# Optimization experiments

Measured on AMD Instinct MI355X. Metric: run time of the kernel, lower is better.

## Reference

```python
import jax, jax.numpy as jnp
import numpy as np

N_HEAD = 16


def setup_inputs() -> dict:
    key = jax.random.key(0)
    ks = jax.random.split(key, 6)
    B, T, H = 4, 2048, 1024
    inp = jax.random.normal(ks[0], (B, T, H), dtype=jnp.float32)
    # padding mask: valid prefix of random length in [T//2, T] per batch row
    lengths = jax.random.randint(ks[1], (B, 1), T // 2, T + 1)
    mask = jnp.arange(T)[None, :] < lengths  # (B, T) bool
    s = 0.02
    w_qkv = jax.random.normal(ks[2], (H, 3 * H), dtype=jnp.float32) * s
    b_qkv = jax.random.normal(ks[3], (3 * H,), dtype=jnp.float32) * s
    w_out = jax.random.normal(ks[4], (H, H), dtype=jnp.float32) * s
    b_out = jax.random.normal(ks[5], (H,), dtype=jnp.float32) * s
    return {"input": inp, "mask": mask, "w_qkv": w_qkv, "b_qkv": b_qkv,
            "w_out": w_out, "b_out": b_out}


def reference(input, mask, w_qkv, b_qkv, w_out, b_out):
    B, T, H = input.shape
    hd = H // N_HEAD
    qkv = input @ w_qkv + b_qkv                       # (B, T, 3H)
    q, k, v = jnp.split(qkv, 3, axis=-1)
    # (B, T, H) -> (B, nh, T, hd)
    q = q.reshape(B, T, N_HEAD, hd).transpose(0, 2, 1, 3)
    k = k.reshape(B, T, N_HEAD, hd).transpose(0, 2, 1, 3)
    v = v.reshape(B, T, N_HEAD, hd).transpose(0, 2, 1, 3)
    scores = jnp.einsum('bhqd,bhkd->bhqk', q, k) / jnp.sqrt(jnp.float32(hd))
    causal = jnp.tril(jnp.ones((T, T), dtype=bool))   # (T, T)
    full_mask = causal[None, None, :, :] & mask[:, None, None, :]  # (B,1,T,T) bcast over heads
    scores = jnp.where(full_mask, scores, -jnp.inf)
    attn = jax.nn.softmax(scores, axis=-1)            # (B, nh, T, T)
    o = jnp.einsum('bhqk,bhkd->bhqd', attn, v)        # (B, nh, T, hd)
    o = o.transpose(0, 2, 1, 3).reshape(B, T, H)
    return o @ w_out + b_out
```

## Files before the change

### kernel.cpp

```cpp
#include <hip/hip_runtime.h>
#include <math.h>

#define B_  4
#define T_  2048
#define H_  1024
#define NH  16
#define HD  64
#define H3  3072

typedef short bf16x8 __attribute__((ext_vector_type(8)));
typedef short bf16x4 __attribute__((ext_vector_type(4)));
typedef float f32x4  __attribute__((ext_vector_type(4)));
typedef float f32x16 __attribute__((ext_vector_type(16)));

#define SC2F 0.18033688011112042f

__device__ __forceinline__ unsigned short f2bf(float f) {
    union { float f; unsigned u; } v; v.f = f;
    unsigned u = v.u;
    unsigned r = (u + 0x7fffu + ((u >> 16) & 1u)) >> 16;
    return (unsigned short)r;
}

__device__ __forceinline__ void gload_lds16(const void* g, void* l) {
    __builtin_amdgcn_global_load_lds(
        (const __attribute__((address_space(1))) unsigned*)g,
        (__attribute__((address_space(3))) unsigned*)l, 16, 0, 0);
}

__device__ __forceinline__ f32x4 mfma_16x16x16_bf16(bf16x4 a, bf16x4 b, f32x4 c) {
#if __has_builtin(__builtin_amdgcn_mfma_f32_16x16x16_bf16)
    return __builtin_amdgcn_mfma_f32_16x16x16_bf16(a, b, c, 0, 0, 0);
#elif __has_builtin(__builtin_amdgcn_mfma_f32_16x16x16bf16_1k)
    return __builtin_amdgcn_mfma_f32_16x16x16bf16_1k(a, b, c, 0, 0, 0);
#else
    f32x4 d;
    asm volatile("v_mfma_f32_16x16x16_bf16 %0, %1, %2, %3"
                 : "=v"(d) : "v"(a), "v"(b), "v"(c));
    return d;
#endif
}

__global__ void lengths_kernel(const void* mask, int* lengths) {
    int b = blockIdx.x;
    int t = threadIdx.x;
    const unsigned* mu = (const unsigned*)mask;
    bool is_byte = (mu[0] == 0x01010101u);
    int cnt = 0;
    if (is_byte) {
        const unsigned char* m8 = (const unsigned char*)mask;
        for (int i = t; i < T_; i += 256) cnt += (m8[b * T_ + i] != 0);
    } else {
        const unsigned* m32 = (const unsigned*)mask;
        for (int i = t; i < T_; i += 256) cnt += (m32[b * T_ + i] != 0);
    }
    __shared__ int red[256];
    red[t] = cnt;
    __syncthreads();
    for (int s = 128; s > 0; s >>= 1) {
        if (t < s) red[t] += red[t + s];
        __syncthreads();
    }
    if (t == 0) lengths[b] = red[0];
}

__global__ void convert_bf16_kernel(const float* __restrict__ x,
                                    unsigned short* __restrict__ y, int n) {
    int i = (blockIdx.x * 256 + threadIdx.x) * 4;
    if (i < n) {
        float4 v = *(const float4*)(x + i);
        ushort4 o;
        o.x = f2bf(v.x); o.y = f2bf(v.y); o.z = f2bf(v.z); o.w = f2bf(v.w);
        *(ushort4*)(y + i) = o;
    }
}

__global__ void transpose2_kernel(const float* __restrict__ Wqkv,
                                  unsigned short* __restrict__ WqkvT,
                                  const float* __restrict__ Wout,
                                  unsigned short* __restrict__ WoutT) {
    __shared__ unsigned short tile[32][33];
    const int K = H_;
    const float* in;
    unsigned short* out;
    int N, nb;
    if (blockIdx.x < 96) { in = Wqkv; out = WqkvT; N = H3; nb = blockIdx.x * 32; }
    else                 { in = Wout; out = WoutT; N = H_; nb = (blockIdx.x - 96) * 32; }
    int kb = blockIdx.y * 32;
    int tx = threadIdx.x, ty = threadIdx.y;
    for (int i = 0; i < 32; i += 8)
        tile[ty + i][tx] = f2bf(in[(long)(kb + ty + i) * N + nb + tx]);
    __syncthreads();
    for (int i = 0; i < 32; i += 8)
        out[(long)(nb + ty + i) * K + kb + tx] = tile[tx][ty + i];
}

template <int TN, bool BF16_OUT, bool KSCALE, bool VSPLIT>
__global__ __launch_bounds__(256) void gemm_kernel(
    const unsigned short* __restrict__ A,
    const unsigned short* __restrict__ Bt,
    const float* __restrict__ bias,
    void* __restrict__ C,
    unsigned short* __restrict__ Vt,
    int M, int N, int K)
{
    __shared__ unsigned short Asm[2][128][64];
    __shared__ unsigned short Bsm[2][TN][64];

    int nbx = gridDim.x;
    int bid = blockIdx.y * nbx + blockIdx.x;
    int cpx = (nbx * gridDim.y) >> 3;
    int lin = (bid & 7) * cpx + (bid >> 3);
    int bx = lin % nbx, by = lin / nbx;

    int tn = bx * TN, tm = by * 128;
    int tid = threadIdx.x;
    int wid = tid >> 6, lane = tid & 63;
    int l31 = lane & 31, lh = lane >> 5;
    int wm = (wid & 1) * 64, wn = (wid >> 1) * (TN / 2);

    int rl = lane >> 3;
    int g8 = ((lane & 7) ^ rl) * 8;
    const unsigned short* aP = A  + (long)(tm + wid * 32 + rl) * K + g8;
    const unsigned short* bP = Bt + (long)(tn + wid * (TN / 4) + rl) * K + g8;
    int rk = l31 & 7;

    f32x16 acc[2][TN / 64] = {};

#pragma unroll
    for (int t = 0; t < 4; t++)
        gload_lds16(aP + (long)(t * 8) * K, &Asm[0][wid * 32 + t * 8][0]);
#pragma unroll
    for (int t = 0; t < TN / 32; t++)
        gload_lds16(bP + (long)(t * 8) * K, &Bsm[0][wid * (TN / 4) + t * 8][0]);

    int cur = 0;
    for (int k0 = 0; k0 < K; k0 += 64) {
        __syncthreads();

        if (k0 + 64 < K) {
#pragma unroll
            for (int t = 0; t < 4; t++)
                gload_lds16(aP + (long)(t * 8) * K + k0 + 64, &Asm[cur ^ 1][wid * 32 + t * 8][0]);
#pragma unroll
            for (int t = 0; t < TN / 32; t++)
                gload_lds16(bP + (long)(t * 8) * K + k0 + 64, &Bsm[cur ^ 1][wid * (TN / 4) + t * 8][0]);
        }

#pragma unroll
        for (int ks = 0; ks < 4; ks++) {
            int pc = ((ks * 2 + lh) ^ rk) * 8;
            bf16x8 af[2], bv[TN / 64];
            af[0] = *(const bf16x8*)(&Asm[cur][wm + l31][pc]);
            af[1] = *(const bf16x8*)(&Asm[cur][wm + 32 + l31][pc]);
#pragma unroll
            for (int j = 0; j < TN / 64; j++)
                bv[j] = *(const bf16x8*)(&Bsm[cur][wn + j * 32 + l31][pc]);
#pragma unroll
            for (int i = 0; i < 2; i++)
#pragma unroll
                for (int j = 0; j < TN / 64; j++)
                    acc[i][j] = __builtin_amdgcn_mfma_f32_32x32x16_bf16(
                        af[i], bv[j], acc[i][j], 0, 0, 0);
        }
        cur ^= 1;
    }

    if (VSPLIT && tn >= 2 * H_) {
#pragma unroll
        for (int i = 0; i < 2; i++)
#pragma unroll
            for (int j = 0; j < TN / 64; j++) {
                int col = tn + wn + j * 32 + l31;
                float bs = bias[col];
                int feat = col - 2 * H_;
#pragma unroll
                for (int rg = 0; rg < 4; rg++) {
                    int tok0 = tm + wm + i * 32 + rg * 8 + lh * 4;
                    int bb = tok0 >> 11;
                    unsigned d0 = (unsigned)f2bf(acc[i][j][rg * 4 + 0] + bs) |
                                  ((unsigned)f2bf(acc[i][j][rg * 4 + 1] + bs) << 16);
                    unsigned d1 = (unsigned)f2bf(acc[i][j][rg * 4 + 2] + bs) |
                                  ((unsigned)f2bf(acc[i][j][rg * 4 + 3] + bs) << 16);
                    unsigned short* dst = Vt + ((long)(bb * 1024 + feat)) * T_ + (tok0 & (T_ - 1));
                    *(uint2*)dst = make_uint2(d0, d1);
                }
            }
        return;
    }

#pragma unroll
    for (int i = 0; i < 2; i++)
#pragma unroll
        for (int j = 0; j < TN / 64; j++) {
            int col = tn + wn + j * 32 + l31;
            float bs = bias[col];
            bool ks_ = KSCALE && (col >= H_) && (col < 2 * H_);
#pragma unroll
            for (int r = 0; r < 16; r++) {
                int row = tm + wm + i * 32 + (r & 3) + 8 * (r >> 2) + 4 * lh;
                float v = acc[i][j][r] + bs;
                if (ks_) v *= SC2F;
                if (BF16_OUT)
                    ((unsigned short*)C)[(long)row * N + col] = f2bf(v);
                else
                    ((float*)C)[(long)row * N + col] = v;
            }
        }
}

__global__ __launch_bounds__(256) void attn_kernel(
    const unsigned short* __restrict__ QKV,
    const unsigned short* __restrict__ Vt,
    const int* __restrict__ lengths,
    unsigned short* __restrict__ O)
{
    int idx = blockIdx.x;
    int bh = idx & 63;
    int qt = 15 - (idx >> 6);
    int b = bh >> 4, h = bh & 15;
    int len = lengths[b];
    int q0 = qt * 128;

    int tid = threadIdx.x;
    int wid = tid >> 6, lane = tid & 63, quad = lane >> 4, lr = lane & 15;
    int quad4 = quad * 4;

    __shared__ __align__(16) unsigned short SH[16384];
    unsigned short (*Kd)[64][64] = (unsigned short (*)[64][64])(&SH[0]);
    unsigned short (*Vd)[64][64] = (unsigned short (*)[64][64])(&SH[8192]);

    const long qkv_base = (long)b * T_ * H3;

    bf16x8 qf[2][2];
#pragma unroll
    for (int nq = 0; nq < 2; nq++)
#pragma unroll
        for (int ks = 0; ks < 2; ks++)
            qf[nq][ks] = *(const bf16x8*)(QKV + qkv_base +
                (long)(q0 + wid * 32 + nq * 16 + lr) * H3 + h * HD + ks * 32 + quad * 8);

    int rl = lane >> 3;
    int g8 = ((lane & 7) ^ rl) * 8;
    const unsigned short* kB = QKV + qkv_base + (long)(wid * 16 + rl) * H3 + H_ + h * HD + g8;
    const unsigned short* vB = Vt + (long)(bh * 64 + wid * 16 + rl) * T_ + g8;

    f32x4 lacc[2] = {};
    f32x4 Oacc[4][2] = {};

    int kmax = min(q0 + 127, len - 1);
    int n_kt = (kmax >> 6) + 1;
    int q_wave_lo = q0 + wid * 32;
    int qwl_u = __builtin_amdgcn_readfirstlane(q_wave_lo);
    int q_wave_hi = qwl_u + 31;
    int bnd_[2] = { min(q_wave_lo + lr, len - 1),
                    min(q_wave_lo + 16 + lr, len - 1) };
    int rk = lr & 7;

    const short oneb = (short)0x3F80;
    bf16x4 vones = { oneb, oneb, oneb, oneb };

#pragma unroll
    for (int t = 0; t < 2; t++) {
        gload_lds16(kB + (long)(t * 8) * H3, &Kd[0][wid * 16 + t * 8][0]);
        gload_lds16(vB + (long)(t * 8) * T_, &Vd[0][wid * 16 + t * 8][0]);
    }

    for (int kt = 0; kt < n_kt; kt++) {
        int cur = kt & 1;
        __syncthreads();

        if (kt + 1 < n_kt) {
            long koff = (long)((kt + 1) * 64) * H3;
            int voff = (kt + 1) * 64;
#pragma unroll
            for (int t = 0; t < 2; t++) {
                gload_lds16(kB + koff + (long)(t * 8) * H3, &Kd[cur ^ 1][wid * 16 + t * 8][0]);
                gload_lds16(vB + (long)(t * 8) * T_ + voff, &Vd[cur ^ 1][wid * 16 + t * 8][0]);
            }
        }

        int k_lo = kt * 64;
        if (k_lo > q_wave_hi || k_lo >= len) continue;

        int mt_hi = min(q_wave_hi, len - 1);
        int nmt = min(4, ((mt_hi - k_lo) >> 4) + 1);
        nmt = __builtin_amdgcn_readfirstlane(nmt);

        f32x4 Sacc[4][2] = {};
        __builtin_amdgcn_s_setprio(1);
#pragma unroll
        for (int mt = 0; mt < 4; mt++) {
            if (mt >= nmt) continue;
#pragma unroll
            for (int ks = 0; ks < 2; ks++) {
                bf16x8 kf = *(const bf16x8*)(&Kd[cur][mt * 16 + lr][((ks * 4 + quad) ^ rk) * 8]);
                Sacc[mt][0] = __builtin_amdgcn_mfma_f32_16x16x32_bf16(kf, qf[0][ks], Sacc[mt][0], 0, 0, 0);
                Sacc[mt][1] = __builtin_amdgcn_mfma_f32_16x16x32_bf16(kf, qf[1][ks], Sacc[mt][1], 0, 0, 0);
            }
        }
        __builtin_amdgcn_s_setprio(0);

        unsigned pkk[4][2][2];
#pragma unroll
        for (int mt = 0; mt < 4; mt++) {
            if (mt >= nmt) continue;
            int kb0 = k_lo + mt * 16;
            int kbl = kb0 + quad4;
#pragma unroll
            for (int nq = 0; nq < 2; nq++) {
                float p[4];
                if (kb0 + 15 <= qwl_u + nq * 16 && kb0 + 15 < len) {
#pragma unroll
                    for (int r = 0; r < 4; r++)
                        p[r] = __builtin_amdgcn_exp2f(Sacc[mt][nq][r]);
                } else {
                    int dlt = bnd_[nq] - kbl;
#pragma unroll
                    for (int r = 0; r < 4; r++) {
                        float s = (r <= dlt) ? Sacc[mt][nq][r] : -INFINITY;
                        p[r] = __builtin_amdgcn_exp2f(s);
                    }
                }
                pkk[mt][nq][0] = __builtin_amdgcn_perm(__float_as_uint(p[1]), __float_as_uint(p[0]), 0x07060302);
                pkk[mt][nq][1] = __builtin_amdgcn_perm(__float_as_uint(p[3]), __float_as_uint(p[2]), 0x07060302);
            }
        }

        __builtin_amdgcn_s_setprio(1);
#pragma unroll
        for (int mt = 0; mt < 4; mt++) {
            if (mt >= nmt) continue;
            union { unsigned u[2]; bf16x4 v; } bu[2];
            bu[0].u[0] = pkk[mt][0][0]; bu[0].u[1] = pkk[mt][0][1];
            bu[1].u[0] = pkk[mt][1][0]; bu[1].u[1] = pkk[mt][1][1];
            lacc[0] = mfma_16x16x16_bf16(vones, bu[0].v, lacc[0]);
            lacc[1] = mfma_16x16x16_bf16(vones, bu[1].v, lacc[1]);
#pragma unroll
            for (int md = 0; md < 4; md++) {
                bf16x4 vf = *(const bf16x4*)(&Vd[cur][md * 16 + lr]
                    [((mt * 2 + (quad >> 1)) ^ rk) * 8 + (quad & 1) * 4]);
                Oacc[md][0] = mfma_16x16x16_bf16(vf, bu[0].v, Oacc[md][0]);
                Oacc[md][1] = mfma_16x16x16_bf16(vf, bu[1].v, Oacc[md][1]);
            }
        }
        __builtin_amdgcn_s_setprio(0);
    }

    __syncthreads();
    {
        unsigned short (*Es)[68] = (unsigned short (*)[68])(&SH[0]);
        float inv[2] = { 1.f / lacc[0][0], 1.f / lacc[1][0] };
#pragma unroll
        for (int nq = 0; nq < 2; nq++)
#pragma unroll
            for (int md = 0; md < 4; md++)
#pragma unroll
                for (int rp = 0; rp < 2; rp++) {
                    float e0 = Oacc[md][nq][rp * 2]     * inv[nq];
                    float e1 = Oacc[md][nq][rp * 2 + 1] * inv[nq];
                    unsigned w = __builtin_amdgcn_perm(__float_as_uint(e1), __float_as_uint(e0), 0x07060302);
                    *(unsigned*)(&Es[wid * 32 + nq * 16 + lr][md * 16 + quad * 4 + rp * 2]) = w;
                }
        __asm__ volatile("s_waitcnt lgkmcnt(0)" ::: "memory");
        int row = lane >> 1, cb = (lane & 1) * 32;
        long tok = (long)b * T_ + q0 + wid * 32 + row;
#pragma unroll
        for (int i = 0; i < 4; i++) {
            float4 v = *(const float4*)(&Es[wid * 32 + row][cb + i * 8]);
            *(float4*)(&O[tok * H_ + h * HD + cb + i * 8]) = v;
        }
    }
}

extern "C" void kernel_launch(void* const* d_in, const int* in_sizes, int n_in,
                              void* d_out, int out_size, void* d_ws, size_t ws_size,
                              hipStream_t stream) {
    const float* X    = (const float*)d_in[0];
    const void*  mask = d_in[1];
    const float* Wqkv = (const float*)d_in[2];
    const float* bqkv = (const float*)d_in[3];
    const float* Wout = (const float*)d_in[4];
    const float* bout = (const float*)d_in[5];

    char* ws = (char*)d_ws;
    int* lengths          = (int*)ws;
    unsigned short* WqkvT = (unsigned short*)(ws + 256);
    unsigned short* WoutT = WqkvT + (long)H3 * H_;
    unsigned short* QKV   = WoutT + (long)H_ * H_;
    unsigned short* Xbf   = QKV + (long)B_ * T_ * H3;
    unsigned short* Vt    = Xbf + (long)B_ * T_ * H_;
    unsigned short* Obf   = Xbf;

    const int M = B_ * T_;

    lengths_kernel<<<B_, 256, 0, stream>>>(mask, lengths);
    convert_bf16_kernel<<<(M * H_ / 4 + 255) / 256, 256, 0, stream>>>(X, Xbf, M * H_);
    transpose2_kernel<<<dim3(128, H_ / 32), dim3(32, 8), 0, stream>>>(Wqkv, WqkvT, Wout, WoutT);
    gemm_kernel<128, true, true, true><<<dim3(H3 / 128, M / 128), 256, 0, stream>>>(
        Xbf, WqkvT, bqkv, QKV, Vt, M, H3, H_);
    attn_kernel<<<B_ * NH * (T_ / 128), 256, 0, stream>>>(QKV, Vt, lengths, Obf);
    gemm_kernel<64, false, false, false><<<dim3(H_ / 64, M / 128), 256, 0, stream>>>(
        Obf, WoutT, bout, d_out, nullptr, M, H_, H_);
}
```

Measured before the change: 269.9 us.

## Add 256x256 ping-pong scheduled GEMM kernel for the QKV projection

Measured after the change: 278.4 us. +3.1%, slower.

```diff
diff --git a/kernel.cpp b/kernel.cpp
--- a/kernel.cpp
+++ b/kernel.cpp
@@ -95,13 +95,151 @@
         out[(long)(nb + ty + i) * K + kb + tx] = tile[tx][ty + i];
 }
 
-template <int TN, bool BF16_OUT, bool KSCALE, bool VSPLIT>
+#define SPRIO1 __builtin_amdgcn_s_setprio(1)
+#define SPRIO0 __builtin_amdgcn_s_setprio(0)
+#define MIDBAR do { __builtin_amdgcn_sched_barrier(0); __builtin_amdgcn_s_barrier(); \
+    asm volatile("s_waitcnt lgkmcnt(0)" ::: "memory"); __builtin_amdgcn_sched_barrier(0); } while (0)
+#define ENDBAR do { __builtin_amdgcn_sched_barrier(0); __builtin_amdgcn_s_barrier(); \
+    __builtin_amdgcn_sched_barrier(0); } while (0)
+
+__global__ __launch_bounds__(512, 2) void gemm256_kernel(
+    const unsigned short* __restrict__ A,
+    const unsigned short* __restrict__ Bt,
+    const float* __restrict__ bias,
+    unsigned short* __restrict__ C,
+    unsigned short* __restrict__ Vt)
+{
+    const int K = 1024;
+    __shared__ unsigned short As[2][128][64];
+    __shared__ unsigned short Bs[2][128][64];
+
+    int bid = blockIdx.y * 12 + blockIdx.x;
+    int lin = (bid & 7) * 48 + (bid >> 3);
+    int bx = lin % 12, by = lin / 12;
+    int tn = bx * 256, tm = by * 256;
+
+    int tid = threadIdx.x;
+    int wid = tid >> 6, lane = tid & 63;
+    int l31 = lane & 31, lh = lane >> 5;
+    int wr = wid >> 2, wc = wid & 3;
+
+    int rl = lane >> 3;
+    int g  = (lane & 7) ^ rl;
+    const unsigned short* aP = A  + (long)(tm + (wid & 3) * 16 + (wid >> 2) * 128
+                                           + 2 * rl + (g >> 2)) * K + (g & 3) * 8;
+    const unsigned short* bP = Bt + (long)(tn + (wid >> 1) * 64 + (wid & 1) * 16
+                                           + 2 * rl + (g >> 2)) * K + (g & 3) * 8;
+    int awb = (wid & 3) * 8 + (wid >> 2) * 64;
+    int bwb = (wid >> 1) * 32 + (wid & 1) * 8;
+
+#define STG_A(bf, mq, kel) gload_lds16(aP + (long)(mq) * 64 * K + (kel), &As[bf][(mq) * 32 + awb][0])
+#define STG_B(bf, nq, kel) gload_lds16(bP + (long)(nq) * 32 * K + (kel), &Bs[bf][(nq) * 16 + bwb][0])
+
+    int rA  = (l31 >> 1) & 7;
+    int pc0 = (((l31 & 1) * 4) + lh) ^ rA;
+    int aR  = wr * 64 + (l31 >> 1);
+    int bR  = wc * 32 + (l31 >> 1);
+
+#define LD_A(dst, bf, mq) do { \
+    dst[0][0] = *(const bf16x8*)(&As[bf][aR + (mq) * 32][pc0 * 8]); \
+    dst[0][1] = *(const bf16x8*)(&As[bf][aR + (mq) * 32][(pc0 ^ 2) * 8]); \
+    dst[1][0] = *(const bf16x8*)(&As[bf][aR + (mq) * 32 + 16][pc0 * 8]); \
+    dst[1][1] = *(const bf16x8*)(&As[bf][aR + (mq) * 32 + 16][(pc0 ^ 2) * 8]); } while (0)
+#define LD_B(dst, bf, nq) do { \
+    dst[0] = *(const bf16x8*)(&Bs[bf][bR + (nq) * 16][pc0 * 8]); \
+    dst[1] = *(const bf16x8*)(&Bs[bf][bR + (nq) * 16][(pc0 ^ 2) * 8]); } while (0)
+#define MM(mq, af_, nq, bv_) do { \
+    _Pragma("unroll") for (int mf = 0; mf < 2; mf++) \
+    _Pragma("unroll") for (int kk = 0; kk < 2; kk++) \
+        acc[mq][mf][nq] = __builtin_amdgcn_mfma_f32_32x32x16_bf16( \
+            af_[mf][kk], bv_[kk], acc[mq][mf][nq], 0, 0, 0); } while (0)
+
+    f32x16 acc[2][2][2] = {};
+
+    STG_A(0, 0, 0); STG_B(0, 0, 0); STG_A(0, 1, 0); STG_B(0, 1, 0);
+    asm volatile("s_waitcnt vmcnt(2)" ::: "memory");
+    __builtin_amdgcn_sched_barrier(0);
+    STG_A(1, 0, 32); STG_B(1, 0, 32); STG_A(1, 1, 32);
+    asm volatile("s_waitcnt vmcnt(3)" ::: "memory");
+    __builtin_amdgcn_sched_barrier(0);
+    __builtin_amdgcn_s_barrier();
+
+    bf16x8 afA[2][2], afB[2][2], bvA[2], bvB[2];
+
+    for (int it = 0; it < 16; ++it) {
+        bool fl = (it < 15);
+        int kE = it * 64;
+        int kO = kE + 32;
+        int kE2 = kE + 64;
+        int kO2 = kE + 96;
+
+        LD_A(afA, 0, 0); LD_B(bvA, 0, 0);
+        STG_B(1, 1, kO);
+        MIDBAR; SPRIO1; MM(0, afA, 0, bvA); SPRIO0; ENDBAR;
+        LD_A(afB, 0, 1);
+        if (fl) STG_A(0, 0, kE2);
+        MIDBAR; SPRIO1; MM(1, afB, 0, bvA); SPRIO0; ENDBAR;
+        LD_B(bvB, 0, 1);
+        if (fl) STG_B(0, 0, kE2);
+        MIDBAR; SPRIO1; MM(0, afA, 1, bvB); SPRIO0; ENDBAR;
+        if (fl) { STG_A(0, 1, kE2); asm volatile("s_waitcnt vmcnt(3)" ::: "memory"); }
+        else    { asm volatile("s_waitcnt vmcnt(0)" ::: "memory"); }
+        MIDBAR; SPRIO1; MM(1, afB, 1, bvB); SPRIO0; ENDBAR;
+        LD_A(afA, 1, 0); LD_B(bvA, 1, 0);
+        if (fl) STG_B(0, 1, kE2);
+        MIDBAR; SPRIO1; MM(0, afA, 0, bvA); SPRIO0; ENDBAR;
+        LD_A(afB, 1, 1);
+        if (fl) STG_A(1, 0, kO2);
+        MIDBAR; SPRIO1; MM(1, afB, 0, bvA); SPRIO0; ENDBAR;
+        LD_B(bvB, 1, 1);
+        if (fl) STG_B(1, 0, kO2);
+        MIDBAR; SPRIO1; MM(0, afA, 1, bvB); SPRIO0; ENDBAR;
+        if (fl) { STG_A(1, 1, kO2); asm volatile("s_waitcnt vmcnt(3)" ::: "memory"); }
+        MIDBAR; SPRIO1; MM(1, afB, 1, bvB); SPRIO0; ENDBAR;
+    }
+
+    bool vsplit = (tn >= 2 * H_);
+#pragma unroll
+    for (int mq = 0; mq < 2; mq++)
+#pragma unroll
+        for (int mf = 0; mf < 2; mf++)
+#pragma unroll
+            for (int nq = 0; nq < 2; nq++) {
+                int col = tn + wc * 64 + nq * 32 + l31;
+                float bs = bias[col];
+                int rbase = tm + wr * 128 + mq * 64 + mf * 32;
+                if (vsplit) {
+                    int feat = col - 2 * H_;
+#pragma unroll
+                    for (int rg = 0; rg < 4; rg++) {
+                        int tok0 = rbase + rg * 8 + lh * 4;
+                        int bb = tok0 >> 11;
+                        unsigned d0 = (unsigned)f2bf(acc[mq][mf][nq][rg * 4 + 0] + bs) |
+                                      ((unsigned)f2bf(acc[mq][mf][nq][rg * 4 + 1] + bs) << 16);
+                        unsigned d1 = (unsigned)f2bf(acc[mq][mf][nq][rg * 4 + 2] + bs) |
+                                      ((unsigned)f2bf(acc[mq][mf][nq][rg * 4 + 3] + bs) << 16);
+                        unsigned short* dst = Vt + ((long)(bb * 1024 + feat)) * T_ + (tok0 & (T_ - 1));
+                        *(uint2*)dst = make_uint2(d0, d1);
+                    }
+                } else {
+                    bool ks_ = (col >= H_) && (col < 2 * H_);
+#pragma unroll
+                    for (int r = 0; r < 16; r++) {
+                        int row = rbase + (r & 3) + 8 * (r >> 2) + 4 * lh;
+                        float v = acc[mq][mf][nq][r] + bs;
+                        if (ks_) v *= SC2F;
+                        C[(long)row * H3 + col] = f2bf(v);
+                    }
+                }
+            }
+}
+
+template <int TN>
 __global__ __launch_bounds__(256) void gemm_kernel(
     const unsigned short* __restrict__ A,
     const unsigned short* __restrict__ Bt,
     const float* __restrict__ bias,
-    void* __restrict__ C,
-    unsigned short* __restrict__ Vt,
+    float* __restrict__ C,
     int M, int N, int K)
 {
     __shared__ unsigned short Asm[2][128][64];
@@ -137,7 +275,6 @@
     int cur = 0;
     for (int k0 = 0; k0 < K; k0 += 64) {
         __syncthreads();
-
         if (k0 + 64 < K) {
 #pragma unroll
             for (int t = 0; t < 4; t++)
@@ -146,7 +283,6 @@
             for (int t = 0; t < TN / 32; t++)
                 gload_lds16(bP + (long)(t * 8) * K + k0 + 64, &Bsm[cur ^ 1][wid * (TN / 4) + t * 8][0]);
         }
-
 #pragma unroll
         for (int ks = 0; ks < 4; ks++) {
             int pc = ((ks * 2 + lh) ^ rk) * 8;
@@ -166,45 +302,16 @@
         cur ^= 1;
     }
 
-    if (VSPLIT && tn >= 2 * H_) {
-#pragma unroll
-        for (int i = 0; i < 2; i++)
-#pragma unroll
-            for (int j = 0; j < TN / 64; j++) {
-                int col = tn + wn + j * 32 + l31;
-                float bs = bias[col];
-                int feat = col - 2 * H_;
-#pragma unroll
-                for (int rg = 0; rg < 4; rg++) {
-                    int tok0 = tm + wm + i * 32 + rg * 8 + lh * 4;
-                    int bb = tok0 >> 11;
-                    unsigned d0 = (unsigned)f2bf(acc[i][j][rg * 4 + 0] + bs) |
-                                  ((unsigned)f2bf(acc[i][j][rg * 4 + 1] + bs) << 16);
-                    unsigned d1 = (unsigned)f2bf(acc[i][j][rg * 4 + 2] + bs) |
-                                  ((unsigned)f2bf(acc[i][j][rg * 4 + 3] + bs) << 16);
-                    unsigned short* dst = Vt + ((long)(bb * 1024 + feat)) * T_ + (tok0 & (T_ - 1));
-                    *(uint2*)dst = make_uint2(d0, d1);
-                }
-            }
-        return;
-    }
-
 #pragma unroll
     for (int i = 0; i < 2; i++)
 #pragma unroll
         for (int j = 0; j < TN / 64; j++) {
             int col = tn + wn + j * 32 + l31;
             float bs = bias[col];
-            bool ks_ = KSCALE && (col >= H_) && (col < 2 * H_);
 #pragma unroll
             for (int r = 0; r < 16; r++) {
                 int row = tm + wm + i * 32 + (r & 3) + 8 * (r >> 2) + 4 * lh;
-                float v = acc[i][j][r] + bs;
-                if (ks_) v *= SC2F;
-                if (BF16_OUT)
-                    ((unsigned short*)C)[(long)row * N + col] = f2bf(v);
-                else
-                    ((float*)C)[(long)row * N + col] = v;
+                C[(long)row * N + col] = acc[i][j][r] + bs;
             }
         }
 }
@@ -397,9 +504,9 @@
     lengths_kernel<<<B_, 256, 0, stream>>>(mask, lengths);
     convert_bf16_kernel<<<(M * H_ / 4 + 255) / 256, 256, 0, stream>>>(X, Xbf, M * H_);
     transpose2_kernel<<<dim3(128, H_ / 32), dim3(32, 8), 0, stream>>>(Wqkv, WqkvT, Wout, WoutT);
-    gemm_kernel<128, true, true, true><<<dim3(H3 / 128, M / 128), 256, 0, stream>>>(
-        Xbf, WqkvT, bqkv, QKV, Vt, M, H3, H_);
+    gemm256_kernel<<<dim3(H3 / 256, M / 256), 512, 0, stream>>>(
+        Xbf, WqkvT, bqkv, QKV, Vt);
     attn_kernel<<<B_ * NH * (T_ / 128), 256, 0, stream>>>(QKV, Vt, lengths, Obf);
-    gemm_kernel<64, false, false, false><<<dim3(H_ / 64, M / 128), 256, 0, stream>>>(
-        Obf, WoutT, bout, d_out, nullptr, M, H_, H_);
-}
+    gemm_kernel<64><<<dim3(H_ / 64, M / 128), 256, 0, stream>>>(
+        Obf, WoutT, bout, (float*)d_out, M, H_, H_);
+}
```

## Merge prep kernels, inline mask length in attention, simplify QKV GEMM

Applied to the files above, without the earlier changes.

Result: no change. 266.2 us, median of 2 (-1.4%).

```diff
diff --git a/kernel.cpp b/kernel.cpp
--- a/kernel.cpp
+++ b/kernel.cpp
@@ -41,136 +41,98 @@
 #endif
 }
 
-__global__ void lengths_kernel(const void* mask, int* lengths) {
-    int b = blockIdx.x;
+__global__ __launch_bounds__(256) void prep_kernel(
+    const float* __restrict__ X, unsigned short* __restrict__ Xbf,
+    const float* __restrict__ Wqkv, unsigned short* __restrict__ WqkvT,
+    const float* __restrict__ Wout, unsigned short* __restrict__ WoutT)
+{
+    int bid = blockIdx.x;
     int t = threadIdx.x;
-    const unsigned* mu = (const unsigned*)mask;
-    bool is_byte = (mu[0] == 0x01010101u);
-    int cnt = 0;
-    if (is_byte) {
-        const unsigned char* m8 = (const unsigned char*)mask;
-        for (int i = t; i < T_; i += 256) cnt += (m8[b * T_ + i] != 0);
+    if (bid < 4096) {
+        __shared__ unsigned short tile[32][33];
+        int bxx = bid & 127, byy = bid >> 7;
+        const float* in;
+        unsigned short* out;
+        int N, nb;
+        if (bxx < 96) { in = Wqkv; out = WqkvT; N = H3; nb = bxx * 32; }
+        else          { in = Wout; out = WoutT; N = H_; nb = (bxx - 96) * 32; }
+        int kb = byy * 32;
+        int tx = t & 31, ty = t >> 5;
+        for (int i = 0; i < 32; i += 8)
+            tile[ty + i][tx] = f2bf(in[(long)(kb + ty + i) * N + nb + tx]);
+        __syncthreads();
+        for (int i = 0; i < 32; i += 8)
+            out[(long)(nb + ty + i) * H_ + kb + tx] = tile[tx][ty + i];
     } else {
-        const unsigned* m32 = (const unsigned*)mask;
-        for (int i = t; i < T_; i += 256) cnt += (m32[b * T_ + i] != 0);
-    }
-    __shared__ int red[256];
-    red[t] = cnt;
-    __syncthreads();
-    for (int s = 128; s > 0; s >>= 1) {
-        if (t < s) red[t] += red[t + s];
-        __syncthreads();
-    }
-    if (t == 0) lengths[b] = red[0];
-}
-
-__global__ void convert_bf16_kernel(const float* __restrict__ x,
-                                    unsigned short* __restrict__ y, int n) {
-    int i = (blockIdx.x * 256 + threadIdx.x) * 4;
-    if (i < n) {
-        float4 v = *(const float4*)(x + i);
-        ushort4 o;
-        o.x = f2bf(v.x); o.y = f2bf(v.y); o.z = f2bf(v.z); o.w = f2bf(v.w);
-        *(ushort4*)(y + i) = o;
-    }
-}
-
-__global__ void transpose2_kernel(const float* __restrict__ Wqkv,
-                                  unsigned short* __restrict__ WqkvT,
-                                  const float* __restrict__ Wout,
-                                  unsigned short* __restrict__ WoutT) {
-    __shared__ unsigned short tile[32][33];
-    const int K = H_;
-    const float* in;
-    unsigned short* out;
-    int N, nb;
-    if (blockIdx.x < 96) { in = Wqkv; out = WqkvT; N = H3; nb = blockIdx.x * 32; }
-    else                 { in = Wout; out = WoutT; N = H_; nb = (blockIdx.x - 96) * 32; }
-    int kb = blockIdx.y * 32;
-    int tx = threadIdx.x, ty = threadIdx.y;
-    for (int i = 0; i < 32; i += 8)
-        tile[ty + i][tx] = f2bf(in[(long)(kb + ty + i) * N + nb + tx]);
-    __syncthreads();
-    for (int i = 0; i < 32; i += 8)
-        out[(long)(nb + ty + i) * K + kb + tx] = tile[tx][ty + i];
-}
-
-template <int TN, bool BF16_OUT, bool KSCALE, bool VSPLIT>
-__global__ __launch_bounds__(256) void gemm_kernel(
+        long u = (long)(bid - 4096) * 256 + t;
+#pragma unroll
+        for (int j = 0; j < 4; j++) {
+            long i = (u + (long)j * 524288) * 4;
+            float4 v = *(const float4*)(X + i);
+            ushort4 o;
+            o.x = f2bf(v.x); o.y = f2bf(v.y); o.z = f2bf(v.z); o.w = f2bf(v.w);
+            *(ushort4*)(Xbf + i) = o;
+        }
+    }
+}
+
+__global__ __launch_bounds__(256) void gemm_qkv_kernel(
     const unsigned short* __restrict__ A,
     const unsigned short* __restrict__ Bt,
     const float* __restrict__ bias,
-    void* __restrict__ C,
-    unsigned short* __restrict__ Vt,
-    int M, int N, int K)
+    unsigned short* __restrict__ C,
+    unsigned short* __restrict__ Vt)
 {
-    __shared__ unsigned short Asm[2][128][64];
-    __shared__ unsigned short Bsm[2][TN][64];
-
-    int nbx = gridDim.x;
-    int bid = blockIdx.y * nbx + blockIdx.x;
-    int cpx = (nbx * gridDim.y) >> 3;
-    int lin = (bid & 7) * cpx + (bid >> 3);
-    int bx = lin % nbx, by = lin / nbx;
-
-    int tn = bx * TN, tm = by * 128;
+    const int K = H_, N = H3;
+    __shared__ unsigned short Asm[128][64];
+    __shared__ unsigned short Bsm[128][64];
+
+    int tn = blockIdx.x * 128, tm = blockIdx.y * 128;
     int tid = threadIdx.x;
     int wid = tid >> 6, lane = tid & 63;
     int l31 = lane & 31, lh = lane >> 5;
-    int wm = (wid & 1) * 64, wn = (wid >> 1) * (TN / 2);
+    int wm = (wid & 1) * 64, wn = (wid >> 1) * 64;
 
     int rl = lane >> 3;
     int g8 = ((lane & 7) ^ rl) * 8;
     const unsigned short* aP = A  + (long)(tm + wid * 32 + rl) * K + g8;
-    const unsigned short* bP = Bt + (long)(tn + wid * (TN / 4) + rl) * K + g8;
+    const unsigned short* bP = Bt + (long)(tn + wid * 32 + rl) * K + g8;
     int rk = l31 & 7;
 
-    f32x16 acc[2][TN / 64] = {};
-
-#pragma unroll
-    for (int t = 0; t < 4; t++)
-        gload_lds16(aP + (long)(t * 8) * K, &Asm[0][wid * 32 + t * 8][0]);
-#pragma unroll
-    for (int t = 0; t < TN / 32; t++)
-        gload_lds16(bP + (long)(t * 8) * K, &Bsm[0][wid * (TN / 4) + t * 8][0]);
-
-    int cur = 0;
+    f32x16 acc[2][2] = {};
+
     for (int k0 = 0; k0 < K; k0 += 64) {
         __syncthreads();
-
-        if (k0 + 64 < K) {
-#pragma unroll
-            for (int t = 0; t < 4; t++)
-                gload_lds16(aP + (long)(t * 8) * K + k0 + 64, &Asm[cur ^ 1][wid * 32 + t * 8][0]);
-#pragma unroll
-            for (int t = 0; t < TN / 32; t++)
-                gload_lds16(bP + (long)(t * 8) * K + k0 + 64, &Bsm[cur ^ 1][wid * (TN / 4) + t * 8][0]);
-        }
+#pragma unroll
+        for (int t = 0; t < 4; t++)
+            gload_lds16(aP + (long)(t * 8) * K + k0, &Asm[wid * 32 + t * 8][0]);
+#pragma unroll
+        for (int t = 0; t < 4; t++)
+            gload_lds16(bP + (long)(t * 8) * K + k0, &Bsm[wid * 32 + t * 8][0]);
+        __syncthreads();
 
 #pragma unroll
         for (int ks = 0; ks < 4; ks++) {
             int pc = ((ks * 2 + lh) ^ rk) * 8;
-            bf16x8 af[2], bv[TN / 64];
-            af[0] = *(const bf16x8*)(&Asm[cur][wm + l31][pc]);
-            af[1] = *(const bf16x8*)(&Asm[cur][wm + 32 + l31][pc]);
-#pragma unroll
-            for (int j = 0; j < TN / 64; j++)
-                bv[j] = *(const bf16x8*)(&Bsm[cur][wn + j * 32 + l31][pc]);
+            bf16x8 af[2], bv[2];
+            af[0] = *(const bf16x8*)(&Asm[wm + l31][pc]);
+            af[1] = *(const bf16x8*)(&Asm[wm + 32 + l31][pc]);
+            bv[0] = *(const bf16x8*)(&Bsm[wn + l31][pc]);
+            bv[1] = *(const bf16x8*)(&Bsm[wn + 32 + l31][pc]);
 #pragma unroll
             for (int i = 0; i < 2; i++)
 #pragma unroll
-                for (int j = 0; j < TN / 64; j++)
+                for (int j = 0; j < 2; j++)
                     acc[i][j] = __builtin_amdgcn_mfma_f32_32x32x16_bf16(
                         af[i], bv[j], acc[i][j], 0, 0, 0);
         }
-        cur ^= 1;
-    }
-
-    if (VSPLIT && tn >= 2 * H_) {
+    }
+
+    if (tn >= 2 * H_) {
 #pragma unroll
         for (int i = 0; i < 2; i++)
 #pragma unroll
-            for (int j = 0; j < TN / 64; j++) {
+            for (int j = 0; j < 2; j++) {
                 int col = tn + wn + j * 32 + l31;
                 float bs = bias[col];
                 int feat = col - 2 * H_;
@@ -192,19 +154,98 @@
 #pragma unroll
     for (int i = 0; i < 2; i++)
 #pragma unroll
-        for (int j = 0; j < TN / 64; j++) {
+        for (int j = 0; j < 2; j++) {
             int col = tn + wn + j * 32 + l31;
             float bs = bias[col];
-            bool ks_ = KSCALE && (col >= H_) && (col < 2 * H_);
+            bool ks_ = (col >= H_) && (col < 2 * H_);
 #pragma unroll
             for (int r = 0; r < 16; r++) {
                 int row = tm + wm + i * 32 + (r & 3) + 8 * (r >> 2) + 4 * lh;
                 float v = acc[i][j][r] + bs;
                 if (ks_) v *= SC2F;
-                if (BF16_OUT)
-                    ((unsigned short*)C)[(long)row * N + col] = f2bf(v);
-                else
-                    ((float*)C)[(long)row * N + col] = v;
+                C[(long)row * N + col] = f2bf(v);
+            }
+        }
+}
+
+template <int TN>
+__global__ __launch_bounds__(256) void gemm_kernel(
+    const unsigned short* __restrict__ A,
+    const unsigned short* __restrict__ Bt,
+    const float* __restrict__ bias,
+    float* __restrict__ C,
+    int M, int N, int K)
+{
+    __shared__ unsigned short Asm[2][128][64];
+    __shared__ unsigned short Bsm[2][TN][64];
+
+    int nbx = gridDim.x;
+    int bid = blockIdx.y * nbx + blockIdx.x;
+    int cpx = (nbx * gridDim.y) >> 3;
+    int lin = (bid & 7) * cpx + (bid >> 3);
+    int bx = lin % nbx, by = lin / nbx;
+
+    int tn = bx * TN, tm = by * 128;
+    int tid = threadIdx.x;
+    int wid = tid >> 6, lane = tid & 63;
+    int l31 = lane & 31, lh = lane >> 5;
+    int wm = (wid & 1) * 64, wn = (wid >> 1) * (TN / 2);
+
+    int rl = lane >> 3;
+    int g8 = ((lane & 7) ^ rl) * 8;
+    const unsigned short* aP = A  + (long)(tm + wid * 32 + rl) * K + g8;
+    const unsigned short* bP = Bt + (long)(tn + wid * (TN / 4) + rl) * K + g8;
+    int rk = l31 & 7;
+
+    f32x16 acc[2][TN / 64] = {};
+
+#pragma unroll
+    for (int t = 0; t < 4; t++)
+        gload_lds16(aP + (long)(t * 8) * K, &Asm[0][wid * 32 + t * 8][0]);
+#pragma unroll
+    for (int t = 0; t < TN / 32; t++)
+        gload_lds16(bP + (long)(t * 8) * K, &Bsm[0][wid * (TN / 4) + t * 8][0]);
+
+    int cur = 0;
+    for (int k0 = 0; k0 < K; k0 += 64) {
+        __syncthreads();
+        if (k0 + 64 < K) {
+#pragma unroll
+            for (int t = 0; t < 4; t++)
+                gload_lds16(aP + (long)(t * 8) * K + k0 + 64, &Asm[cur ^ 1][wid * 32 + t * 8][0]);
+#pragma unroll
+            for (int t = 0; t < TN / 32; t++)
+                gload_lds16(bP + (long)(t * 8) * K + k0 + 64, &Bsm[cur ^ 1][wid * (TN / 4) + t * 8][0]);
+        }
+#pragma unroll
+        for (int ks = 0; ks < 4; ks++) {
+            int pc = ((ks * 2 + lh) ^ rk) * 8;
+            bf16x8 af[2], bv[TN / 64];
+            af[0] = *(const bf16x8*)(&Asm[cur][wm + l31][pc]);
+            af[1] = *(const bf16x8*)(&Asm[cur][wm + 32 + l31][pc]);
+#pragma unroll
+            for (int j = 0; j < TN / 64; j++)
+                bv[j] = *(const bf16x8*)(&Bsm[cur][wn + j * 32 + l31][pc]);
+#pragma unroll
+            for (int i = 0; i < 2; i++)
+#pragma unroll
+                for (int j = 0; j < TN / 64; j++)
+                    acc[i][j] = __builtin_amdgcn_mfma_f32_32x32x16_bf16(
+                        af[i], bv[j], acc[i][j], 0, 0, 0);
+        }
+        cur ^= 1;
+    }
+
+#pragma unroll
+    for (int i = 0; i < 2; i++)
+#pragma unroll
+        for (int j = 0; j < TN / 64; j++) {
+            int col = tn + wn + j * 32 + l31;
+            float bs = bias[col];
+#pragma unroll
+            for (int r = 0; r < 16; r++) {
+                int row = tm + wm + i * 32 + (r & 3) + 8 * (r >> 2) + 4 * lh;
+                C[(long)row * N + col] = acc[i][j][r] + bs;
             }
         }
 }
@@ -212,19 +253,36 @@
 __global__ __launch_bounds__(256) void attn_kernel(
     const unsigned short* __restrict__ QKV,
     const unsigned short* __restrict__ Vt,
-    const int* __restrict__ lengths,
+    const void* __restrict__ mask,
     unsigned short* __restrict__ O)
 {
     int idx = blockIdx.x;
     int bh = idx & 63;
     int qt = 15 - (idx >> 6);
     int b = bh >> 4, h = bh & 15;
-    int len = lengths[b];
     int q0 = qt * 128;
 
     int tid = threadIdx.x;
     int wid = tid >> 6, lane = tid & 63, quad = lane >> 4, lr = lane & 15;
     int quad4 = quad * 4;
+
+    int len;
+    {
+        const unsigned* mu = (const unsigned*)mask;
+        bool is_byte = (mu[0] == 0x01010101u);
+        int cnt = 0;
+        if (is_byte) {
+            const unsigned char* m8 = (const unsigned char*)mask;
+            for (int i = lane; i < T_; i += 64) cnt += (m8[b * T_ + i] != 0);
+        } else {
+            const unsigned* m32 = (const unsigned*)mask;
+            for (int i = lane; i < T_; i += 64) cnt += (m32[b * T_ + i] != 0);
+        }
+        cnt += __shfl_xor(cnt, 1);  cnt += __shfl_xor(cnt, 2);
+        cnt += __shfl_xor(cnt, 4);  cnt += __shfl_xor(cnt, 8);
+        cnt += __shfl_xor(cnt, 16); cnt += __shfl_xor(cnt, 32);
+        len = cnt;
+    }
 
     __shared__ __align__(16) unsigned short SH[16384];
     unsigned short (*Kd)[64][64] = (unsigned short (*)[64][64])(&SH[0]);
@@ -384,7 +442,6 @@
     const float* bout = (const float*)d_in[5];
 
     char* ws = (char*)d_ws;
-    int* lengths          = (int*)ws;
     unsigned short* WqkvT = (unsigned short*)(ws + 256);
     unsigned short* WoutT = WqkvT + (long)H3 * H_;
     unsigned short* QKV   = WoutT + (long)H_ * H_;
@@ -394,12 +451,10 @@
 
     const int M = B_ * T_;
 
-    lengths_kernel<<<B_, 256, 0, stream>>>(mask, lengths);
-    convert_bf16_kernel<<<(M * H_ / 4 + 255) / 256, 256, 0, stream>>>(X, Xbf, M * H_);
-    transpose2_kernel<<<dim3(128, H_ / 32), dim3(32, 8), 0, stream>>>(Wqkv, WqkvT, Wout, WoutT);
-    gemm_kernel<128, true, true, true><<<dim3(H3 / 128, M / 128), 256, 0, stream>>>(
-        Xbf, WqkvT, bqkv, QKV, Vt, M, H3, H_);
-    attn_kernel<<<B_ * NH * (T_ / 128), 256, 0, stream>>>(QKV, Vt, lengths, Obf);
-    gemm_kernel<64, false, false, false><<<dim3(H_ / 64, M / 128), 256, 0, stream>>>(
-        Obf, WoutT, bout, d_out, nullptr, M, H_, H_);
-}
+    prep_kernel<<<6144, 256, 0, stream>>>(X, Xbf, Wqkv, WqkvT, Wout, WoutT);
+    gemm_qkv_kernel<<<dim3(H3 / 128, M / 128), 256, 0, stream>>>(
+        Xbf, WqkvT, bqkv, QKV, Vt);
+    attn_kernel<<<B_ * NH * (T_ / 128), 256, 0, stream>>>(QKV, Vt, mask, Obf);
+    gemm_kernel<64><<<dim3(H_ / 64, M / 128), 256, 0, stream>>>(
+        Obf, WoutT, bout, (float*)d_out, M, H_, H_);
+}
```
